# Performance work log

Measured on AMD Instinct MI355X. Metric: run time of the kernel, lower is better.

## Reference

```python
import jax, jax.numpy as jnp
import numpy as np

D_MODEL = 1024
D_STATE = 64
D_CONV = 4
EXPAND = 2
D_INNER = D_MODEL * EXPAND


def setup_inputs() -> dict:
    key = jax.random.key(0)
    ks = jax.random.split(key, 12)
    s = lambda *sh: 1.0 / np.sqrt(sh[-1])
    x = jax.random.normal(ks[0], (2, 2048, D_MODEL), dtype=jnp.float32)
    in_proj_w = jax.random.normal(ks[1], (2 * D_INNER, D_MODEL), dtype=jnp.float32) * s(D_MODEL)
    in_proj_b = jax.random.normal(ks[2], (2 * D_INNER,), dtype=jnp.float32) * 0.01
    conv_w = jax.random.normal(ks[3], (D_INNER, 1, D_CONV), dtype=jnp.float32) * s(D_CONV)
    conv_b = jax.random.normal(ks[4], (D_INNER,), dtype=jnp.float32) * 0.01
    # S4 params match nn.Parameter(torch.randn(...)) but scaled to keep tanh scan stable
    A = jax.random.normal(ks[5], (D_STATE, D_STATE), dtype=jnp.float32) * s(D_STATE)
    B = jax.random.normal(ks[6], (D_STATE, D_INNER), dtype=jnp.float32) * s(D_INNER)
    C = jax.random.normal(ks[7], (D_INNER, D_STATE), dtype=jnp.float32) * s(D_STATE)
    D = jax.random.normal(ks[8], (D_INNER,), dtype=jnp.float32)
    out_proj_w = jax.random.normal(ks[9], (D_MODEL, D_INNER), dtype=jnp.float32) * s(D_INNER)
    out_proj_b = jax.random.normal(ks[10], (D_MODEL,), dtype=jnp.float32) * 0.01
    return {"x": x, "in_proj_w": in_proj_w, "in_proj_b": in_proj_b,
            "conv_w": conv_w, "conv_b": conv_b,
            "A": A, "B": B, "C": C, "D": D,
            "out_proj_w": out_proj_w, "out_proj_b": out_proj_b}


def _mamba_fwd(x, in_proj_w, in_proj_b, conv_w, conv_b, A, B, C, D, out_proj_w, out_proj_b):
    bsz, seq_len, _ = x.shape
    # in_proj: (b, s, 2*d_inner)
    x_proj = jnp.einsum('bsd,ed->bse', x, in_proj_w) + in_proj_b
    x_ssm, x_gate = jnp.split(x_proj, 2, axis=-1)
    # causal depthwise conv1d: pad left (d_conv-1), no right pad (== torch pad both + slice[:seq_len])
    lhs = jnp.transpose(x_ssm, (0, 2, 1))  # (b, d_inner, s)
    x_conv = jax.lax.conv_general_dilated(
        lhs, conv_w, window_strides=(1,), padding=[(D_CONV - 1, 0)],
        dimension_numbers=('NCH', 'OIH', 'NCH'), feature_group_count=D_INNER)
    x_conv = jnp.transpose(x_conv + conv_b[None, :, None], (0, 2, 1))  # (b, s, d_inner)
    x_conv = jax.nn.silu(x_conv)
    # S4 tanh recurrence over time via lax.scan
    xs = jnp.transpose(x_conv, (1, 0, 2))  # (s, b, d_inner)
    h0 = jnp.zeros((bsz, D_STATE), dtype=x.dtype)

    def step(h, xt):
        h = jnp.tanh(h @ A.T + xt @ B.T)          # (b, d_state)
        y = h @ C.T + xt * D                       # (b, d_inner)
        return h, y

    _, ys = jax.lax.scan(step, h0, xs)
    x_ssm_out = jnp.transpose(ys, (1, 0, 2))       # (b, s, d_inner)
    x_out = x_ssm_out * jax.nn.silu(x_gate)
    return jnp.einsum('bse,de->bsd', x_out, out_proj_w) + out_proj_b


def reference(x, in_proj_w, in_proj_b, conv_w, conv_b, A, B, C, D, out_proj_w, out_proj_b):
    return _mamba_fwd(x, in_proj_w, in_proj_b, conv_w, conv_b, A, B, C, D, out_proj_w, out_proj_b)
```

## Files before the change

kernel.cpp:

```cpp
#include <hip/hip_runtime.h>
#include <math.h>

#define D_MODEL 1024
#define D_INNER 2048
#define D_STATE 64
#define SEQ     2048
#define BATCH   2
#define NROWS   (BATCH*SEQ)

typedef unsigned short ushort_t;
typedef unsigned int uint_t;

__device__ __forceinline__ float silu_f(float x) { return x / (1.f + __expf(-x)); }
__device__ __forceinline__ ushort_t f2bf(float f) {
    uint_t u = __float_as_uint(f);
    uint_t r = (u + 0x7FFFu + ((u >> 16) & 1u)) >> 16;
    return (ushort_t)r;
}
__device__ __forceinline__ float bf2f(ushort_t u) {
    return __uint_as_float(((uint_t)u) << 16);
}

typedef __attribute__((address_space(1))) const void gvoid_t;
typedef __attribute__((address_space(3))) void lvoid_t;

template<int N> __device__ __forceinline__ void wait_vmcnt() {
    if constexpr (N == 0)      asm volatile("s_waitcnt vmcnt(0)" ::: "memory");
    else if constexpr (N == 3) asm volatile("s_waitcnt vmcnt(3)" ::: "memory");
    else if constexpr (N == 6) asm volatile("s_waitcnt vmcnt(6)" ::: "memory");
    else static_assert(N == 0, "unsupported vmcnt");
}

__global__ __launch_bounds__(256) void cvt5_kernel(
    const float* __restrict__ s0, ushort_t* __restrict__ d0, int b0,
    const float* __restrict__ s1, ushort_t* __restrict__ d1, int b1,
    const float* __restrict__ s2, ushort_t* __restrict__ d2, int b2,
    const float* __restrict__ s3, ushort_t* __restrict__ d3, int b3,
    const float* __restrict__ s4, ushort_t* __restrict__ d4, int b4)
{
    int blk = blockIdx.x;
    const float* s; ushort_t* d;
    if (blk < b0)                    { s = s0; d = d0; }
    else if (blk < b0 + b1)          { s = s1; d = d1; blk -= b0; }
    else if (blk < b0 + b1 + b2)     { s = s2; d = d2; blk -= b0 + b1; }
    else if (blk < b0 + b1 + b2 + b3){ s = s3; d = d3; blk -= b0 + b1 + b2; }
    else                             { s = s4; d = d4; blk -= b0 + b1 + b2 + b3; }
    int i = (blk * 256 + threadIdx.x) * 4;
    float4 v = *reinterpret_cast<const float4*>(s + i);
    ushort4 o;
    o.x = f2bf(v.x); o.y = f2bf(v.y); o.z = f2bf(v.z); o.w = f2bf(v.w);
    *reinterpret_cast<ushort4*>(d + i) = o;
}

__global__ __launch_bounds__(512, 4) void gemm_pipe8_inproj(
    const ushort_t* __restrict__ Abf, const ushort_t* __restrict__ Wbf,
    const float* __restrict__ bias,
    ushort_t* __restrict__ out_x, ushort_t* __restrict__ out_g, int K)
{
    using bf16x8 = __attribute__((ext_vector_type(8))) short;
    using f32x4  = __attribute__((ext_vector_type(4))) float;

    constexpr int BMt  = 256, BNt = 128, BKt = 32;
    constexpr int ABLK = BMt / 16;
    constexpr int NBLK = (BMt + BNt) / 16;
    constexpr int TILE = (BMt + BNt) * BKt;
    constexpr int L    = NBLK / 8;

    __shared__ ushort_t buf[2][TILE];

    const int tid  = threadIdx.x;
    const int lane = tid & 63;
    const int wid  = tid >> 6;
    const int bm   = blockIdx.y * BMt;
    const int bn   = blockIdx.x * BNt;
    const int wr   = (wid >> 1) * 64;
    const int wc   = (wid & 1) * 64;
    const int r16  = lane & 15;
    const int g    = lane >> 4;
    const int srow = lane >> 2;
    const int scg  = ((lane & 3) ^ (srow & 3)) * 8;
    const int rg   = (g ^ (r16 & 3)) * 8;

    f32x4 acc[4][4] = {};

    auto stage = [&](int p, int k0) {
        #pragma unroll
        for (int i = wid; i < NBLK; i += 8) {
            const ushort_t* gsrc;
            if (i < ABLK)
                gsrc = Abf + (size_t)(bm + 16 * i + srow) * K + k0 + scg;
            else
                gsrc = Wbf + (size_t)(bn + 16 * (i - ABLK) + srow) * K + k0 + scg;
            __builtin_amdgcn_global_load_lds((gvoid_t*)gsrc, (lvoid_t*)(&buf[p][i * 512]), 16, 0, 0);
        }
    };

    const int NT = K / BKt;
    stage(0, 0);
    stage(1, BKt);
    wait_vmcnt<L>();
    __builtin_amdgcn_s_barrier();

    for (int t = 0; t < NT; ++t) {
        const ushort_t* Tb = &buf[t & 1][0];
        bf16x8 af[4], bfr[4];
        #pragma unroll
        for (int m = 0; m < 4; ++m)
            af[m] = *reinterpret_cast<const bf16x8*>(
                &Tb[((wr >> 4) + m) * 512 + r16 * 32 + rg]);
        #pragma unroll
        for (int n = 0; n < 4; ++n)
            bfr[n] = *reinterpret_cast<const bf16x8*>(
                &Tb[(ABLK + (wc >> 4) + n) * 512 + r16 * 32 + rg]);

        asm volatile("s_waitcnt lgkmcnt(0)" ::: "memory");
        __builtin_amdgcn_s_barrier();

        if (t + 2 < NT) stage(t & 1, (t + 2) * BKt);

        #pragma unroll
        for (int m = 0; m < 4; ++m)
            #pragma unroll
            for (int n = 0; n < 4; ++n)
                acc[m][n] = __builtin_amdgcn_mfma_f32_16x16x32_bf16(af[m], bfr[n], acc[m][n], 0, 0, 0);

        if (t + 1 < NT) {
            if (t + 2 < NT) wait_vmcnt<L>();
            else            wait_vmcnt<0>();
            __builtin_amdgcn_s_barrier();
        }
    }

    #pragma unroll
    for (int m = 0; m < 4; ++m) {
        int row0 = bm + wr + m * 16 + g * 4;
        #pragma unroll
        for (int n = 0; n < 4; ++n) {
            int col = bn + wc + n * 16 + r16;
            float b = bias[col];
            if (col < D_INNER) {
                #pragma unroll
                for (int jj = 0; jj < 4; ++jj)
                    out_x[(size_t)(row0 + jj) * D_INNER + col] = f2bf(acc[m][n][jj] + b);
            } else {
                int c2 = col - D_INNER;
                #pragma unroll
                for (int jj = 0; jj < 4; ++jj)
                    out_g[(size_t)(row0 + jj) * D_INNER + c2] = f2bf(silu_f(acc[m][n][jj] + b));
            }
        }
    }
}

template <int BMt, int BNt, int KH>
__global__ __launch_bounds__(256) void gemm_pipe(
    const ushort_t* __restrict__ Abf, const ushort_t* __restrict__ Wbf,
    const float* __restrict__ bias,
    float* __restrict__ out0, int M, int N, int K)
{
    using bf16x8 = __attribute__((ext_vector_type(8))) short;
    using f32x4  = __attribute__((ext_vector_type(4))) float;

    constexpr int BKt  = 32 * KH;
    constexpr int MF   = BMt / 32;
    constexpr int NF   = BNt / 32;
    constexpr int ARB  = BMt / 16;
    constexpr int BRB  = BNt / 16;
    constexpr int ABLK = ARB * KH;
    constexpr int NBLK = (ARB + BRB) * KH;
    constexpr int TILE = (BMt + BNt) * BKt;
    constexpr int L    = NBLK / 4;

    __shared__ ushort_t buf[2][TILE];

    const int tid  = threadIdx.x;
    const int lane = tid & 63;
    const int wid  = tid >> 6;

    const int nbn  = N / BNt;
    const int bid  = blockIdx.x;
    const int nb   = (M / BMt) * nbn;
    const int cpx  = nb / 8;
    const int flat = (bid & 7) * cpx + (bid >> 3);
    const int bm   = (flat / nbn) * BMt;
    const int bn   = (flat % nbn) * BNt;

    const int wr   = (wid >> 1) * (BMt / 2);
    const int wc   = (wid & 1) * (BNt / 2);
    const int r16  = lane & 15;
    const int g    = lane >> 4;
    const int srow = lane >> 2;
    const int scg  = ((lane & 3) ^ (srow & 3)) * 8;
    const int rg   = (g ^ (r16 & 3)) * 8;

    f32x4 acc[MF][NF] = {};

    auto stage = [&](int p, int k0) {
        #pragma unroll
        for (int i = wid; i < NBLK; i += 4) {
            const ushort_t* gsrc;
            if (i < ABLK) {
                int kh = i / ARB, rb = i % ARB;
                gsrc = Abf + (size_t)(bm + 16 * rb + srow) * K + k0 + kh * 32 + scg;
            } else {
                int j = i - ABLK;
                int kh = j / BRB, rb = j % BRB;
                gsrc = Wbf + (size_t)(bn + 16 * rb + srow) * K + k0 + kh * 32 + scg;
            }
            __builtin_amdgcn_global_load_lds((gvoid_t*)gsrc, (lvoid_t*)(&buf[p][i * 512]), 16, 0, 0);
        }
    };

    const int NT = K / BKt;
    stage(0, 0);
    stage(1, BKt);
    wait_vmcnt<L>();
    __builtin_amdgcn_s_barrier();

    for (int t = 0; t < NT; ++t) {
        const ushort_t* Tb = &buf[t & 1][0];
        bf16x8 af[MF][KH], bfr[NF][KH];
        #pragma unroll
        for (int kk = 0; kk < KH; ++kk) {
            #pragma unroll
            for (int m = 0; m < MF; ++m)
                af[m][kk] = *reinterpret_cast<const bf16x8*>(
                    &Tb[(kk * ARB + (wr >> 4) + m) * 512 + r16 * 32 + rg]);
            #pragma unroll
            for (int n = 0; n < NF; ++n)
                bfr[n][kk] = *reinterpret_cast<const bf16x8*>(
                    &Tb[(ABLK + kk * BRB + (wc >> 4) + n) * 512 + r16 * 32 + rg]);
        }

        asm volatile("s_waitcnt lgkmcnt(0)" ::: "memory");
        __builtin_amdgcn_s_barrier();

        if (t + 2 < NT) stage(t & 1, (t + 2) * BKt);

        #pragma unroll
        for (int kk = 0; kk < KH; ++kk)
            #pragma unroll
            for (int m = 0; m < MF; ++m)
                #pragma unroll
                for (int n = 0; n < NF; ++n)
                    acc[m][n] = __builtin_amdgcn_mfma_f32_16x16x32_bf16(
                        af[m][kk], bfr[n][kk], acc[m][n], 0, 0, 0);

        if (t + 1 < NT) {
            if (t + 2 < NT) wait_vmcnt<L>();
            else            wait_vmcnt<0>();
            __builtin_amdgcn_s_barrier();
        }
    }

    #pragma unroll
    for (int m = 0; m < MF; ++m) {
        int row0 = bm + wr + m * 16 + g * 4;
        #pragma unroll
        for (int n = 0; n < NF; ++n) {
            int col = bn + wc + n * 16 + r16;
            float b = bias[col];
            #pragma unroll
            for (int jj = 0; jj < 4; ++jj)
                out0[(size_t)(row0 + jj) * N + col] = acc[m][n][jj] + b;
        }
    }
}

__global__ __launch_bounds__(256) void conv_silu4_kernel(
    const ushort_t* __restrict__ xssm,
    const float* __restrict__ conv_w,
    const float* __restrict__ conv_b,
    ushort_t* __restrict__ xc)
{
    int idx = blockIdx.x * 256 + threadIdx.x;
    int cg = idx & (D_INNER / 4 - 1);
    int rg = idx >> 9;
    int c  = cg * 4;
    int r4 = rg * 4;
    int s4 = r4 & (SEQ - 1);

    float4 wv[4];
    #pragma unroll
    for (int cc = 0; cc < 4; ++cc)
        wv[cc] = *reinterpret_cast<const float4*>(conv_w + (c + cc) * 4);
    float4 bv = *reinterpret_cast<const float4*>(conv_b + c);
    float bias[4] = {bv.x, bv.y, bv.z, bv.w};

    float xin[7][4];
    #pragma unroll
    for (int rr = 0; rr < 7; ++rr) {
        if (s4 > 0 || rr >= 3) {
            ushort4 v = *reinterpret_cast<const ushort4*>(xssm + (size_t)(r4 + rr - 3) * D_INNER + c);
            xin[rr][0] = bf2f(v.x); xin[rr][1] = bf2f(v.y);
            xin[rr][2] = bf2f(v.z); xin[rr][3] = bf2f(v.w);
        } else {
            xin[rr][0] = xin[rr][1] = xin[rr][2] = xin[rr][3] = 0.f;
        }
    }

    #pragma unroll
    for (int i = 0; i < 4; ++i) {
        float acc[4] = {bias[0], bias[1], bias[2], bias[3]};
        #pragma unroll
        for (int dt = 0; dt < 4; ++dt) {
            int rr = i + 3 - dt;
            acc[0] += (&wv[0].x)[3 - dt] * xin[rr][0];
            acc[1] += (&wv[1].x)[3 - dt] * xin[rr][1];
            acc[2] += (&wv[2].x)[3 - dt] * xin[rr][2];
            acc[3] += (&wv[3].x)[3 - dt] * xin[rr][3];
        }
        ushort4 h;
        h.x = f2bf(silu_f(acc[0]));
        h.y = f2bf(silu_f(acc[1]));
        h.z = f2bf(silu_f(acc[2]));
        h.w = f2bf(silu_f(acc[3]));
        *reinterpret_cast<ushort4*>(xc + (size_t)(r4 + i) * D_INNER + c) = h;
    }
}

#define BK 32
__global__ __launch_bounds__(128) void xb_mfma(
    const ushort_t* __restrict__ xc, const ushort_t* __restrict__ Bw,
    float* __restrict__ xb)
{
    using bf16x8 = __attribute__((ext_vector_type(8))) short;
    using f32x4  = __attribute__((ext_vector_type(4))) float;

    __shared__ ushort_t As[32 * BK];
    __shared__ ushort_t Bs[64 * BK];

    const int tid  = threadIdx.x;
    const int lane = tid & 63;
    const int wid  = tid >> 6;
    const int bm   = blockIdx.x * 32;
    const int r16  = lane & 15;
    const int g    = lane >> 4;
    const int srow = lane >> 2;
    const int scol = (lane & 3) * 8;

    f32x4 acc[4] = {};

    for (int k0 = 0; k0 < D_INNER; k0 += BK) {
        const ushort_t* ga = xc + (size_t)(bm + 16 * wid + srow) * D_INNER + k0 + scol;
        __builtin_amdgcn_global_load_lds((gvoid_t*)ga, (lvoid_t*)(As + wid * 512), 16, 0, 0);
        #pragma unroll
        for (int ii = 0; ii < 2; ++ii) {
            int i = wid * 2 + ii;
            const ushort_t* gb = Bw + (size_t)(16 * i + srow) * D_INNER + k0 + scol;
            __builtin_amdgcn_global_load_lds((gvoid_t*)gb, (lvoid_t*)(Bs + i * 512), 16, 0, 0);
        }
        __syncthreads();

        bf16x8 a = *reinterpret_cast<const bf16x8*>(&As[(wid * 16 + r16) * BK + g * 8]);
        #pragma unroll
        for (int n = 0; n < 4; ++n) {
            bf16x8 bv = *reinterpret_cast<const bf16x8*>(&Bs[(n * 16 + r16) * BK + g * 8]);
            acc[n] = __builtin_amdgcn_mfma_f32_16x16x32_bf16(a, bv, acc[n], 0, 0, 0);
        }
        __syncthreads();
    }

    #pragma unroll
    for (int n = 0; n < 4; ++n) {
        int col  = n * 16 + r16;
        int row0 = bm + wid * 16 + g * 4;
        #pragma unroll
        for (int jj = 0; jj < 4; ++jj)
            xb[(size_t)(row0 + jj) * D_STATE + col] = acc[n][jj];
    }
}

#define SCAN_C 32
#define SCAN_W 32
#define NCHUNK (SEQ / SCAN_C)

__global__ __launch_bounds__(64) void scan_kernel(const float* __restrict__ xb,
                                                  const float* __restrict__ A,
                                                  ushort_t* __restrict__ hall)
{
    using f32x4 = __attribute__((ext_vector_type(4))) float;

    __shared__ float xs[(SCAN_C + SCAN_W) * D_STATE];
    __shared__ float hs[D_STATE];

    const int blk = blockIdx.x;
    const int b = blk >> 6;
    const int c = blk & (NCHUNK - 1);
    const int j = threadIdx.x;

    const int t0     = (c == 0) ? 0 : (c * SCAN_C - SCAN_W);
    const int warm   = c * SCAN_C - t0;
    const int nsteps = warm + SCAN_C;

    f32x4 areg[16];
    {
        const f32x4* arow = reinterpret_cast<const f32x4*>(A + j * D_STATE);
        #pragma unroll
        for (int q = 0; q < 16; ++q) areg[q] = arow[q];
    }

    const float* src = xb   + ((size_t)b * SEQ + t0) * D_STATE;
    ushort_t*    dst = hall + ((size_t)b * SEQ + c * SCAN_C) * D_STATE;

    const int nld = nsteps * D_STATE / 256;
    for (int i = 0; i < nld; ++i)
        __builtin_amdgcn_global_load_lds((gvoid_t*)(src + i * 256 + j * 4),
                                         (lvoid_t*)(&xs[i * 256]), 16, 0, 0);
    asm volatile("s_waitcnt vmcnt(0)" ::: "memory");

    hs[j] = 0.f;
    float h = 0.f;
    const f32x4* hp = reinterpret_cast<const f32x4*>(hs);

#define SCAN_STEP(t)                                                     \
    {                                                                    \
        float xv = xs[(t) * D_STATE + j];                                \
        f32x4 a0 = {xv, 0.f, 0.f, 0.f}, a1 = {0.f, 0.f, 0.f, 0.f};      \
        _Pragma("unroll")                                                \
        for (int q = 0; q < 16; q += 2) {                                \
            a0 += areg[q + 0] * hp[q + 0];                               \
            a1 += areg[q + 1] * hp[q + 1];                               \
        }                                                                \
        f32x4 s4 = a0 + a1;                                              \
        float s = (s4[0] + s4[1]) + (s4[2] + s4[3]);                     \
        float e = __expf(2.f * s);                                       \
        h = 1.f - 2.f * __builtin_amdgcn_rcpf(e + 1.f);                  \
        hs[j] = h;                                                       \
    }

    for (int t = 0; t < warm; ++t) {
        SCAN_STEP(t);
    }
    for (int t = warm; t < nsteps; ++t) {
        SCAN_STEP(t);
        dst[(size_t)(t - warm) * D_STATE + j] = f2bf(h);
    }
#undef SCAN_STEP
}

__global__ __launch_bounds__(256) void ymul_mfma(
    const ushort_t* __restrict__ Hbf,
    const ushort_t* __restrict__ Cbf,
    const float* __restrict__ Dv,
    const ushort_t* __restrict__ xc,
    const ushort_t* __restrict__ xg,
    ushort_t* __restrict__ xout)
{
    using bf16x8 = __attribute__((ext_vector_type(8))) short;
    using f32x4  = __attribute__((ext_vector_type(4))) float;

    constexpr int ARB  = 8;
    constexpr int ABLK = 16;
    constexpr int NBLK = 32;

    __shared__ ushort_t Tb[NBLK * 512];

    const int tid  = threadIdx.x;
    const int lane = tid & 63;
    const int wid  = tid >> 6;
    const int bm   = blockIdx.y * 128;
    const int bn   = blockIdx.x * 128;
    const int wr   = (wid >> 1) * 64;
    const int wc   = (wid & 1) * 64;
    const int r16  = lane & 15;
    const int g    = lane >> 4;
    const int srow = lane >> 2;
    const int scg  = ((lane & 3) ^ (srow & 3)) * 8;
    const int rg   = (g ^ (r16 & 3)) * 8;

    #pragma unroll
    for (int i = wid; i < NBLK; i += 4) {
        const ushort_t* gsrc;
        if (i < ABLK) {
            int kh = i / ARB, rb = i % ARB;
            gsrc = Hbf + (size_t)(bm + 16 * rb + srow) * D_STATE + kh * 32 + scg;
        } else {
            int j = i - ABLK;
            int kh = j / ARB, rb = j % ARB;
            gsrc = Cbf + (size_t)(bn + 16 * rb + srow) * D_STATE + kh * 32 + scg;
        }
        __builtin_amdgcn_global_load_lds((gvoid_t*)gsrc, (lvoid_t*)(&Tb[i * 512]), 16, 0, 0);
    }
    __syncthreads();

    f32x4 acc[4][4] = {};
    bf16x8 af[4][2], bfr[4][2];
    #pragma unroll
    for (int kk = 0; kk < 2; ++kk) {
        #pragma unroll
        for (int m = 0; m < 4; ++m)
            af[m][kk] = *reinterpret_cast<const bf16x8*>(
                &Tb[(kk * ARB + (wr >> 4) + m) * 512 + r16 * 32 + rg]);
        #pragma unroll
        for (int n = 0; n < 4; ++n)
            bfr[n][kk] = *reinterpret_cast<const bf16x8*>(
                &Tb[(ABLK + kk * ARB + (wc >> 4) + n) * 512 + r16 * 32 + rg]);
    }
    #pragma unroll
    for (int kk = 0; kk < 2; ++kk)
        #pragma unroll
        for (int m = 0; m < 4; ++m)
            #pragma unroll
            for (int n = 0; n < 4; ++n)
                acc[m][n] = __builtin_amdgcn_mfma_f32_16x16x32_bf16(
                    af[m][kk], bfr[n][kk], acc[m][n], 0, 0, 0);

    #pragma unroll
    for (int m = 0; m < 4; ++m) {
        int row0 = bm + wr + m * 16 + g * 4;
        #pragma unroll
        for (int n = 0; n < 4; ++n) {
            int col = bn + wc + n * 16 + r16;
            float dv = Dv[col];
            #pragma unroll
            for (int jj = 0; jj < 4; ++jj) {
                size_t idx = (size_t)(row0 + jj) * D_INNER + col;
                float y = acc[m][n][jj] + bf2f(xc[idx]) * dv;
                xout[idx] = f2bf(y * bf2f(xg[idx]));
            }
        }
    }
}

extern "C" void kernel_launch(void* const* d_in, const int* in_sizes, int n_in,
                              void* d_out, int out_size, void* d_ws, size_t ws_size,
                              hipStream_t stream)
{
    const float* x          = (const float*)d_in[0];
    const float* in_proj_w  = (const float*)d_in[1];
    const float* in_proj_b  = (const float*)d_in[2];
    const float* conv_w     = (const float*)d_in[3];
    const float* conv_b     = (const float*)d_in[4];
    const float* A          = (const float*)d_in[5];
    const float* B          = (const float*)d_in[6];
    const float* C          = (const float*)d_in[7];
    const float* D          = (const float*)d_in[8];
    const float* out_proj_w = (const float*)d_in[9];
    const float* out_proj_b = (const float*)d_in[10];
    float* out = (float*)d_out;

    char* ws = (char*)d_ws;
    ushort_t* xg_bf   = (ushort_t*)(ws + 0);
    ushort_t* xc_bf   = (ushort_t*)(ws + 16777216);
    ushort_t* xssm_bf = (ushort_t*)(ws + 33554432);
    ushort_t* x_bf    = (ushort_t*)(ws + 50331648);
    ushort_t* w1_bf   = (ushort_t*)(ws + 58720256);
    ushort_t* xout_bf = (ushort_t*)(ws + 50331648);
    ushort_t* w2_bf   = (ushort_t*)(ws + 67108864);
    ushort_t* B_bf    = (ushort_t*)(ws + 71303168);
    float*    xb      = (float*)(ws + 71565312);
    ushort_t* hall_bf = (ushort_t*)(ws + 72613888);
    ushort_t* C_bf    = (ushort_t*)(ws + 73138176);

    {
        int b0 = NROWS * D_MODEL / 1024;
        int b1 = 2 * D_INNER * D_MODEL / 1024;
        int b2 = D_MODEL * D_INNER / 1024;
        int b3 = D_STATE * D_INNER / 1024;
        int b4 = D_INNER * D_STATE / 1024;
        cvt5_kernel<<<b0 + b1 + b2 + b3 + b4, 256, 0, stream>>>(
            x, x_bf, b0, in_proj_w, w1_bf, b1, out_proj_w, w2_bf, b2,
            B, B_bf, b3, C, C_bf, b4);
    }
    {
        dim3 grid(2 * D_INNER / 128, NROWS / 256);
        gemm_pipe8_inproj<<<grid, 512, 0, stream>>>(x_bf, w1_bf, in_proj_b,
                                                    xssm_bf, xg_bf, D_MODEL);
    }
    conv_silu4_kernel<<<NROWS * D_INNER / 16 / 256, 256, 0, stream>>>(xssm_bf, conv_w, conv_b, xc_bf);
    xb_mfma<<<NROWS / 32, 128, 0, stream>>>(xc_bf, B_bf, xb);
    scan_kernel<<<BATCH * NCHUNK, 64, 0, stream>>>(xb, A, hall_bf);
    {
        dim3 grid(D_INNER / 128, NROWS / 128);
        ymul_mfma<<<grid, 256, 0, stream>>>(hall_bf, C_bf, D, xc_bf, xg_bf, xout_bf);
    }
    gemm_pipe<128, 64, 2><<<(NROWS / 128) * (D_MODEL / 64), 256, 0, stream>>>(
        xout_bf, w2_bf, out_proj_b, out, NROWS, D_MODEL, D_INNER);
}
```

Measured before the change: 148.2 us.

## Split in_proj GEMM and co-schedule gate half with fused conv+xB kernel

The in_proj GEMM is split into two launches. The first computes only the x_ssm half with 128x128 tiles. The second launch fuses the gate half's GEMM blocks with new blocks that compute the causal conv+SiLU on the fly and feed the xB MFMA product, which removes the separate conv and xb kernels and the extra round trip of xc. This lets gate GEMM work overlap with the memory-bound conv/xB work. In exchange the tiles shrink from 256x128, the conv reads four shifted rows per element with no reuse, and the xB part uses a simple non-pipelined loop.

```diff
diff --git a/kernel.cpp b/kernel.cpp
--- a/kernel.cpp
+++ b/kernel.cpp
@@ -10,6 +10,7 @@
 
 typedef unsigned short ushort_t;
 typedef unsigned int uint_t;
+typedef __attribute__((ext_vector_type(8))) unsigned short ushort8_t;
 
 __device__ __forceinline__ float silu_f(float x) { return x / (1.f + __expf(-x)); }
 __device__ __forceinline__ ushort_t f2bf(float f) {
@@ -26,6 +27,7 @@
 
 template<int N> __device__ __forceinline__ void wait_vmcnt() {
     if constexpr (N == 0)      asm volatile("s_waitcnt vmcnt(0)" ::: "memory");
+    else if constexpr (N == 2) asm volatile("s_waitcnt vmcnt(2)" ::: "memory");
     else if constexpr (N == 3) asm volatile("s_waitcnt vmcnt(3)" ::: "memory");
     else if constexpr (N == 6) asm volatile("s_waitcnt vmcnt(6)" ::: "memory");
     else static_assert(N == 0, "unsupported vmcnt");
@@ -52,38 +54,38 @@
     *reinterpret_cast<ushort4*>(d + i) = o;
 }
 
-__global__ __launch_bounds__(512, 4) void gemm_pipe8_inproj(
+__device__ __forceinline__ void gemm128_body(
     const ushort_t* __restrict__ Abf, const ushort_t* __restrict__ Wbf,
     const float* __restrict__ bias,
-    ushort_t* __restrict__ out_x, ushort_t* __restrict__ out_g, int K)
+    ushort_t* __restrict__ out_x, ushort_t* __restrict__ out_g,
+    int bm, int bn, ushort_t* smem_u)
 {
     using bf16x8 = __attribute__((ext_vector_type(8))) short;
     using f32x4  = __attribute__((ext_vector_type(4))) float;
 
-    constexpr int BMt  = 256, BNt = 128, BKt = 32;
-    constexpr int ABLK = BMt / 16;
-    constexpr int NBLK = (BMt + BNt) / 16;
-    constexpr int TILE = (BMt + BNt) * BKt;
-    constexpr int L    = NBLK / 8;
-
-    __shared__ ushort_t buf[2][TILE];
+    constexpr int K    = D_MODEL;
+    constexpr int ABLK = 8;
+    constexpr int NBLK = 16;
+    constexpr int TILE = 8192;
+    constexpr int L    = 2;
+
+    ushort_t* buf0 = smem_u;
+    ushort_t* buf1 = smem_u + TILE;
 
     const int tid  = threadIdx.x;
     const int lane = tid & 63;
     const int wid  = tid >> 6;
-    const int bm   = blockIdx.y * BMt;
-    const int bn   = blockIdx.x * BNt;
-    const int wr   = (wid >> 1) * 64;
-    const int wc   = (wid & 1) * 64;
+    const int wr   = (wid >> 2) * 64;
+    const int wc   = (wid & 3) * 32;
     const int r16  = lane & 15;
     const int g    = lane >> 4;
     const int srow = lane >> 2;
     const int scg  = ((lane & 3) ^ (srow & 3)) * 8;
     const int rg   = (g ^ (r16 & 3)) * 8;
 
-    f32x4 acc[4][4] = {};
-
-    auto stage = [&](int p, int k0) {
+    f32x4 acc[4][2] = {};
+
+    auto stage = [&](ushort_t* bufp, int k0) {
         #pragma unroll
         for (int i = wid; i < NBLK; i += 8) {
             const ushort_t* gsrc;
@@ -91,37 +93,37 @@
                 gsrc = Abf + (size_t)(bm + 16 * i + srow) * K + k0 + scg;
             else
                 gsrc = Wbf + (size_t)(bn + 16 * (i - ABLK) + srow) * K + k0 + scg;
-            __builtin_amdgcn_global_load_lds((gvoid_t*)gsrc, (lvoid_t*)(&buf[p][i * 512]), 16, 0, 0);
+            __builtin_amdgcn_global_load_lds((gvoid_t*)gsrc, (lvoid_t*)(bufp + i * 512), 16, 0, 0);
         }
     };
 
-    const int NT = K / BKt;
-    stage(0, 0);
-    stage(1, BKt);
+    const int NT = K / 32;
+    stage(buf0, 0);
+    stage(buf1, 32);
     wait_vmcnt<L>();
     __builtin_amdgcn_s_barrier();
 
     for (int t = 0; t < NT; ++t) {
-        const ushort_t* Tb = &buf[t & 1][0];
-        bf16x8 af[4], bfr[4];
+        const ushort_t* Tb = (t & 1) ? buf1 : buf0;
+        bf16x8 af[4], bfr[2];
         #pragma unroll
         for (int m = 0; m < 4; ++m)
             af[m] = *reinterpret_cast<const bf16x8*>(
                 &Tb[((wr >> 4) + m) * 512 + r16 * 32 + rg]);
         #pragma unroll
-        for (int n = 0; n < 4; ++n)
+        for (int n = 0; n < 2; ++n)
             bfr[n] = *reinterpret_cast<const bf16x8*>(
                 &Tb[(ABLK + (wc >> 4) + n) * 512 + r16 * 32 + rg]);
 
         asm volatile("s_waitcnt lgkmcnt(0)" ::: "memory");
         __builtin_amdgcn_s_barrier();
 
-        if (t + 2 < NT) stage(t & 1, (t + 2) * BKt);
+        if (t + 2 < NT) stage((t & 1) ? buf1 : buf0, (t + 2) * 32);
 
         #pragma unroll
         for (int m = 0; m < 4; ++m)
             #pragma unroll
-            for (int n = 0; n < 4; ++n)
+            for (int n = 0; n < 2; ++n)
                 acc[m][n] = __builtin_amdgcn_mfma_f32_16x16x32_bf16(af[m], bfr[n], acc[m][n], 0, 0, 0);
 
         if (t + 1 < NT) {
@@ -135,7 +137,7 @@
     for (int m = 0; m < 4; ++m) {
         int row0 = bm + wr + m * 16 + g * 4;
         #pragma unroll
-        for (int n = 0; n < 4; ++n) {
+        for (int n = 0; n < 2; ++n) {
             int col = bn + wc + n * 16 + r16;
             float b = bias[col];
             if (col < D_INNER) {
@@ -152,6 +154,117 @@
     }
 }
 
+__global__ __launch_bounds__(512, 4) void gemm_x_half(
+    const ushort_t* __restrict__ Abf, const ushort_t* __restrict__ Wbf,
+    const float* __restrict__ bias,
+    ushort_t* __restrict__ out_x, ushort_t* __restrict__ out_g)
+{
+    __shared__ ushort_t smem_u[16384];
+    gemm128_body(Abf, Wbf, bias, out_x, out_g,
+                 blockIdx.y * 128, blockIdx.x * 128, smem_u);
+}
+
+#define NGEMM 512
+
+__global__ __launch_bounds__(512, 4) void fused_gate_xbconv(
+    const ushort_t* __restrict__ Abf, const ushort_t* __restrict__ Wbf,
+    const float* __restrict__ bias,
+    ushort_t* __restrict__ out_x, ushort_t* __restrict__ out_g,
+    const ushort_t* __restrict__ xssm,
+    const float* __restrict__ conv_w, const float* __restrict__ conv_b,
+    const ushort_t* __restrict__ Bw,
+    ushort_t* __restrict__ xc, float* __restrict__ xb)
+{
+    using bf16x8 = __attribute__((ext_vector_type(8))) short;
+    using f32x4  = __attribute__((ext_vector_type(4))) float;
+
+    __shared__ ushort_t smem_u[16384];
+
+    const int bid = blockIdx.x;
+    if (bid < NGEMM) {
+        const int bm = (bid >> 4) * 128;
+        const int bn = D_INNER + (bid & 15) * 128;
+        gemm128_body(Abf, Wbf, bias, out_x, out_g, bm, bn, smem_u);
+        return;
+    }
+
+    const int bm   = (bid - NGEMM) * 64;
+    const int tid  = threadIdx.x;
+    const int lane = tid & 63;
+    const int w    = tid >> 6;
+    const int wr2  = w >> 1;
+    const int wc2  = w & 1;
+    const int r16  = lane & 15;
+    const int g    = lane >> 4;
+
+    ushort_t* As = smem_u;
+    ushort_t* Bs = smem_u + 2048;
+
+    const bool isA = (tid < 256);
+    const int rl = (isA ? tid : tid - 256) >> 2;
+    const int ck = ((isA ? tid : tid - 256) & 3) * 8;
+
+    const int row = bm + rl;
+    const int s   = row & (SEQ - 1);
+
+    f32x4 acc[2] = {};
+
+    for (int k0 = 0; k0 < D_INNER; k0 += 32) {
+        if (isA) {
+            const int c0 = k0 + ck;
+            float xr[4][8];
+            #pragma unroll
+            for (int dt = 0; dt < 4; ++dt) {
+                if (dt == 0 || s >= dt) {
+                    ushort8_t v = *reinterpret_cast<const ushort8_t*>(
+                        xssm + (size_t)(row - dt) * D_INNER + c0);
+                    #pragma unroll
+                    for (int j = 0; j < 8; ++j) xr[dt][j] = bf2f(v[j]);
+                } else {
+                    #pragma unroll
+                    for (int j = 0; j < 8; ++j) xr[dt][j] = 0.f;
+                }
+            }
+            ushort8_t h;
+            #pragma unroll
+            for (int j = 0; j < 8; ++j) {
+                const float* wv = conv_w + (c0 + j) * 4;
+                float a = conv_b[c0 + j];
+                a += wv[3] * xr[0][j];
+                a += wv[2] * xr[1][j];
+                a += wv[1] * xr[2][j];
+                a += wv[0] * xr[3][j];
+                h[j] = f2bf(silu_f(a));
+            }
+            *reinterpret_cast<ushort8_t*>(As + rl * 32 + ck) = h;
+            *reinterpret_cast<ushort8_t*>(xc + (size_t)row * D_INNER + c0) = h;
+        } else {
+            const ushort_t* gsrc = Bw + (size_t)rl * D_INNER + k0 + ck;
+            __builtin_amdgcn_global_load_lds((gvoid_t*)gsrc,
+                (lvoid_t*)(Bs + (tid - 256) * 8), 16, 0, 0);
+        }
+        __syncthreads();
+
+        bf16x8 a = *reinterpret_cast<const bf16x8*>(&As[(wr2 * 16 + r16) * 32 + g * 8]);
+        #pragma unroll
+        for (int n = 0; n < 2; ++n) {
+            bf16x8 bv = *reinterpret_cast<const bf16x8*>(
+                &Bs[(wc2 * 32 + n * 16 + r16) * 32 + g * 8]);
+            acc[n] = __builtin_amdgcn_mfma_f32_16x16x32_bf16(a, bv, acc[n], 0, 0, 0);
+        }
+        __syncthreads();
+    }
+
+    #pragma unroll
+    for (int n = 0; n < 2; ++n) {
+        int col  = wc2 * 32 + n * 16 + r16;
+        int row0 = bm + wr2 * 16 + g * 4;
+        #pragma unroll
+        for (int jj = 0; jj < 4; ++jj)
+            xb[(size_t)(row0 + jj) * D_STATE + col] = acc[n][jj];
+    }
+}
+
 template <int BMt, int BNt, int KH>
 __global__ __launch_bounds__(256) void gemm_pipe(
     const ushort_t* __restrict__ Abf, const ushort_t* __restrict__ Wbf,
@@ -264,110 +377,6 @@
             for (int jj = 0; jj < 4; ++jj)
                 out0[(size_t)(row0 + jj) * N + col] = acc[m][n][jj] + b;
         }
-    }
-}
-
-__global__ __launch_bounds__(256) void conv_silu4_kernel(
-    const ushort_t* __restrict__ xssm,
-    const float* __restrict__ conv_w,
-    const float* __restrict__ conv_b,
-    ushort_t* __restrict__ xc)
-{
-    int idx = blockIdx.x * 256 + threadIdx.x;
-    int cg = idx & (D_INNER / 4 - 1);
-    int rg = idx >> 9;
-    int c  = cg * 4;
-    int r4 = rg * 4;
-    int s4 = r4 & (SEQ - 1);
-
-    float4 wv[4];
-    #pragma unroll
-    for (int cc = 0; cc < 4; ++cc)
-        wv[cc] = *reinterpret_cast<const float4*>(conv_w + (c + cc) * 4);
-    float4 bv = *reinterpret_cast<const float4*>(conv_b + c);
-    float bias[4] = {bv.x, bv.y, bv.z, bv.w};
-
-    float xin[7][4];
-    #pragma unroll
-    for (int rr = 0; rr < 7; ++rr) {
-        if (s4 > 0 || rr >= 3) {
-            ushort4 v = *reinterpret_cast<const ushort4*>(xssm + (size_t)(r4 + rr - 3) * D_INNER + c);
-            xin[rr][0] = bf2f(v.x); xin[rr][1] = bf2f(v.y);
-            xin[rr][2] = bf2f(v.z); xin[rr][3] = bf2f(v.w);
-        } else {
-            xin[rr][0] = xin[rr][1] = xin[rr][2] = xin[rr][3] = 0.f;
-        }
-    }
-
-    #pragma unroll
-    for (int i = 0; i < 4; ++i) {
-        float acc[4] = {bias[0], bias[1], bias[2], bias[3]};
-        #pragma unroll
-        for (int dt = 0; dt < 4; ++dt) {
-            int rr = i + 3 - dt;
-            acc[0] += (&wv[0].x)[3 - dt] * xin[rr][0];
-            acc[1] += (&wv[1].x)[3 - dt] * xin[rr][1];
-            acc[2] += (&wv[2].x)[3 - dt] * xin[rr][2];
-            acc[3] += (&wv[3].x)[3 - dt] * xin[rr][3];
-        }
-        ushort4 h;
-        h.x = f2bf(silu_f(acc[0]));
-        h.y = f2bf(silu_f(acc[1]));
-        h.z = f2bf(silu_f(acc[2]));
-        h.w = f2bf(silu_f(acc[3]));
-        *reinterpret_cast<ushort4*>(xc + (size_t)(r4 + i) * D_INNER + c) = h;
-    }
-}
-
-#define BK 32
-__global__ __launch_bounds__(128) void xb_mfma(
-    const ushort_t* __restrict__ xc, const ushort_t* __restrict__ Bw,
-    float* __restrict__ xb)
-{
-    using bf16x8 = __attribute__((ext_vector_type(8))) short;
-    using f32x4  = __attribute__((ext_vector_type(4))) float;
-
-    __shared__ ushort_t As[32 * BK];
-    __shared__ ushort_t Bs[64 * BK];
-
-    const int tid  = threadIdx.x;
-    const int lane = tid & 63;
-    const int wid  = tid >> 6;
-    const int bm   = blockIdx.x * 32;
-    const int r16  = lane & 15;
-    const int g    = lane >> 4;
-    const int srow = lane >> 2;
-    const int scol = (lane & 3) * 8;
-
-    f32x4 acc[4] = {};
-
-    for (int k0 = 0; k0 < D_INNER; k0 += BK) {
-        const ushort_t* ga = xc + (size_t)(bm + 16 * wid + srow) * D_INNER + k0 + scol;
-        __builtin_amdgcn_global_load_lds((gvoid_t*)ga, (lvoid_t*)(As + wid * 512), 16, 0, 0);
-        #pragma unroll
-        for (int ii = 0; ii < 2; ++ii) {
-            int i = wid * 2 + ii;
-            const ushort_t* gb = Bw + (size_t)(16 * i + srow) * D_INNER + k0 + scol;
-            __builtin_amdgcn_global_load_lds((gvoid_t*)gb, (lvoid_t*)(Bs + i * 512), 16, 0, 0);
-        }
-        __syncthreads();
-
-        bf16x8 a = *reinterpret_cast<const bf16x8*>(&As[(wid * 16 + r16) * BK + g * 8]);
-        #pragma unroll
-        for (int n = 0; n < 4; ++n) {
-            bf16x8 bv = *reinterpret_cast<const bf16x8*>(&Bs[(n * 16 + r16) * BK + g * 8]);
-            acc[n] = __builtin_amdgcn_mfma_f32_16x16x32_bf16(a, bv, acc[n], 0, 0, 0);
-        }
-        __syncthreads();
-    }
-
-    #pragma unroll
-    for (int n = 0; n < 4; ++n) {
-        int col  = n * 16 + r16;
-        int row0 = bm + wid * 16 + g * 4;
-        #pragma unroll
-        for (int jj = 0; jj < 4; ++jj)
-            xb[(size_t)(row0 + jj) * D_STATE + col] = acc[n][jj];
     }
 }
 
@@ -564,12 +573,12 @@
             B, B_bf, b3, C, C_bf, b4);
     }
     {
-        dim3 grid(2 * D_INNER / 128, NROWS / 256);
-        gemm_pipe8_inproj<<<grid, 512, 0, stream>>>(x_bf, w1_bf, in_proj_b,
-                                                    xssm_bf, xg_bf, D_MODEL);
-    }
-    conv_silu4_kernel<<<NROWS * D_INNER / 16 / 256, 256, 0, stream>>>(xssm_bf, conv_w, conv_b, xc_bf);
-    xb_mfma<<<NROWS / 32, 128, 0, stream>>>(xc_bf, B_bf, xb);
+        dim3 grid(D_INNER / 128, NROWS / 128);
+        gemm_x_half<<<grid, 512, 0, stream>>>(x_bf, w1_bf, in_proj_b, xssm_bf, xg_bf);
+    }
+    fused_gate_xbconv<<<NGEMM + NROWS / 64, 512, 0, stream>>>(
+        x_bf, w1_bf, in_proj_b, xssm_bf, xg_bf,
+        xssm_bf, conv_w, conv_b, B_bf, xc_bf, xb);
     scan_kernel<<<BATCH * NCHUNK, 64, 0, stream>>>(xb, A, hall_bf);
     {
         dim3 grid(D_INNER / 128, NROWS / 128);
```

Result: slower. 261.3 us (+76.3%).
